# Kernel tuning notes

Hardware: AMD Instinct MI355X
Metric: run time of the kernel (lower is better)

Reference implementation:

```python
import jax, jax.numpy as jnp
import numpy as np

N_NODES = 100000


def gcn_conv(x, W, b, edge_index, n):
    """PyG-style GCNConv: x' = D^-1/2 (A+I) D^-1/2 (x W) + b."""
    loop = jnp.arange(n, dtype=edge_index.dtype)
    src = jnp.concatenate([edge_index[0], loop])
    dst = jnp.concatenate([edge_index[1], loop])
    deg = jax.ops.segment_sum(jnp.ones_like(dst, dtype=x.dtype), dst, num_segments=n)
    dinv = jax.lax.rsqrt(deg)  # deg >= 1 because of self-loops
    norm = dinv[src] * dinv[dst]  # [E+N]
    h = x @ W  # [N, out]
    msg = h[src] * norm[:, None]  # gather + scale
    return jax.ops.segment_sum(msg, dst, num_segments=n) + b


def edge_logits(z, edge_index, We, be):
    # concat(src_emb, dst_emb) @ We + be, without materializing the concat twice
    d = z.shape[1]
    return z[edge_index[0]] @ We[:d] + z[edge_index[1]] @ We[d:] + be


def setup_inputs() -> dict:
    key = jax.random.key(0)
    ks = jax.random.split(key, 10)
    x = jax.random.normal(ks[0], (N_NODES, 512), dtype=jnp.float32)
    edge_index = jax.random.randint(ks[1], (2, 3200000), 0, N_NODES, dtype=jnp.int64)
    pos_edge_index = jax.random.randint(ks[2], (2, 1000000), 0, N_NODES, dtype=jnp.int64)
    neg_edge_index = jax.random.randint(ks[3], (2, 1000000), 0, N_NODES, dtype=jnp.int64)
    s1 = 1.0 / np.sqrt(512)
    s2 = 1.0 / np.sqrt(16)
    se = 1.0 / np.sqrt(128)
    W1 = jax.random.uniform(ks[4], (512, 16), jnp.float32, -s1, s1)
    b1 = jnp.zeros((16,), jnp.float32)
    W2 = jax.random.uniform(ks[5], (16, 64), jnp.float32, -s2, s2)
    b2 = jnp.zeros((64,), jnp.float32)
    We = jax.random.uniform(ks[6], (128, 1), jnp.float32, -se, se)  # 2*num_classes -> 1
    be = jnp.zeros((1,), jnp.float32)
    return {"x": x, "W1": W1, "b1": b1, "W2": W2, "b2": b2, "We": We, "be": be,
            "edge_index": edge_index, "pos_edge_index": pos_edge_index,
            "neg_edge_index": neg_edge_index}


def reference(x, W1, b1, W2, b2, We, be, edge_index, pos_edge_index, neg_edge_index):
    n = x.shape[0]
    h = jax.nn.relu(gcn_conv(x, W1, b1, edge_index, n))
    z = gcn_conv(h, W2, b2, edge_index, n)  # node embeddings [N, num_classes]
    pos = edge_logits(z, pos_edge_index, We, be)
    neg = edge_logits(z, neg_edge_index, We, be)
    return z, jnp.concatenate([pos, neg], axis=0)
```

## Files before the change

kernel.cpp:

```cpp
#include <hip/hip_runtime.h>
#include <hip/hip_bf16.h>
#include <hip/hip_fp16.h>


constexpr int TPB = 256;
constexpr int LOG_W = 7;
constexpr int W_BKT = 128;
constexpr int NB_MAX = 1024;
constexpr int CAP = 5120;
constexpr int EPB = 8192;

__global__ __launch_bounds__(256) void scatterA_kernel(const int* __restrict__ src,
                                                       const int* __restrict__ dst,
                                                       int* __restrict__ bcursor,
                                                       int* __restrict__ pairs,
                                                       int E, int NB) {
    __shared__ int hist[NB_MAX];
    __shared__ int lstart[NB_MAX];
    __shared__ int gbase[NB_MAX];
    __shared__ int lcur[NB_MAX];
    __shared__ int csum[256];
    __shared__ int val[EPB];
    __shared__ unsigned short bkt[EPB];
    const int t = threadIdx.x;
    const int e0 = blockIdx.x * EPB;
    const int cnt = min(EPB, E - e0);

    for (int i = t; i < NB; i += 256) hist[i] = 0;
    __syncthreads();
    for (int i = t; i < cnt; i += 256) atomicAdd(&hist[dst[e0 + i] >> LOG_W], 1);
    __syncthreads();

    int loc[4], tsum = 0;
#pragma unroll
    for (int j = 0; j < 4; ++j) {
        int idx = t * 4 + j;
        int v = (idx < NB) ? hist[idx] : 0;
        loc[j] = tsum; tsum += v;
    }
    csum[t] = tsum;
    __syncthreads();
    for (int off = 1; off < 256; off <<= 1) {
        int v = (t >= off) ? csum[t - off] : 0;
        __syncthreads();
        csum[t] += v;
        __syncthreads();
    }
    int cbase = (t > 0) ? csum[t - 1] : 0;
#pragma unroll
    for (int j = 0; j < 4; ++j) {
        int idx = t * 4 + j;
        if (idx < NB) lstart[idx] = cbase + loc[j];
    }
    __syncthreads();
    for (int b = t; b < NB; b += 256) {
        gbase[b] = hist[b] ? atomicAdd(&bcursor[b], hist[b]) : 0;
        lcur[b] = lstart[b];
    }
    __syncthreads();
    for (int i = t; i < cnt; i += 256) {
        int s = src[e0 + i], d = dst[e0 + i];
        int b = d >> LOG_W;
        int p = atomicAdd(&lcur[b], 1);
        val[p] = ((d & (W_BKT - 1)) << 17) | s;
        bkt[p] = (unsigned short)b;
    }
    __syncthreads();
    for (int i = t; i < cnt; i += 256) {
        int b = bkt[i];
        int ofs = gbase[b] + (i - lstart[b]);
        if (ofs < CAP) pairs[(size_t)b * CAP + ofs] = val[i];
    }
}

__global__ __launch_bounds__(256) void bucketB_kernel(const int* __restrict__ bcursor,
                                                      int* __restrict__ pairs,
                                                      float* __restrict__ dinv,
                                                      int* __restrict__ row_start,
                                                      int* __restrict__ row_end,
                                                      int N) {
    __shared__ int cnt[W_BKT];
    __shared__ int scn[W_BKT];
    __shared__ int cur[W_BKT];
    __shared__ int img[CAP];
    const int b = blockIdx.x;
    const int t = threadIdx.x;
    const int len = min(bcursor[b], CAP);
    const int n0 = b * W_BKT;
    int* p = pairs + (size_t)b * CAP;

    if (t < W_BKT) cnt[t] = 0;
    __syncthreads();
    for (int i = t; i < len; i += 256) atomicAdd(&cnt[p[i] >> 17], 1);
    __syncthreads();
    if (t < W_BKT) scn[t] = cnt[t];
    __syncthreads();
    for (int off = 1; off < W_BKT; off <<= 1) {
        int v = (t < W_BKT && t >= off) ? scn[t - off] : 0;
        __syncthreads();
        if (t < W_BKT) scn[t] += v;
        __syncthreads();
    }
    if (t < W_BKT) {
        int c = cnt[t];
        int es = scn[t] - c;
        cur[t] = es;
        int n = n0 + t;
        if (n < N) {
            dinv[n] = rsqrtf((float)(c + 1));
            int rs = b * CAP + es;
            row_start[n] = rs;
            row_end[n] = rs + c;
        }
    }
    __syncthreads();
    for (int i = t; i < len; i += 256) {
        int v = p[i];
        int r = atomicAdd(&cur[v >> 17], 1);
        img[r] = v & 0x1FFFF;
    }
    __syncthreads();
    for (int i = t; i < len; i += 256) p[i] = img[i];
}

__global__ __launch_bounds__(256) void gemm1_kernel(const float* __restrict__ x,
                                                    const float* __restrict__ W1,
                                                    const float* __restrict__ dinv,
                                                    __half* __restrict__ xs, int N) {
    __shared__ float buf[512 * 16];
    const int t = threadIdx.x;
    {
        const float4* w4 = (const float4*)W1;
        float4* b4 = (float4*)buf;
        for (int i = t; i < 2048; i += 256) b4[i] = w4[i];
    }
    __syncthreads();

    const int r = t & 63, q = t >> 6;
    const int row = blockIdx.x * 64 + r;
    const bool valid = row < N;
    const float* xrow = x + (size_t)row * 512 + q * 128;

    float acc[16];
#pragma unroll
    for (int c = 0; c < 16; ++c) acc[c] = 0.0f;

    if (valid) {
        const int kb = q * 128;
#pragma unroll 2
        for (int k0 = 0; k0 < 128; k0 += 16) {
            const float4* xp = (const float4*)(xrow + k0);
            float4 a0 = xp[0], a1 = xp[1], a2 = xp[2], a3 = xp[3];
            float xv[16] = {a0.x, a0.y, a0.z, a0.w, a1.x, a1.y, a1.z, a1.w,
                            a2.x, a2.y, a2.z, a2.w, a3.x, a3.y, a3.z, a3.w};
#pragma unroll
            for (int kk = 0; kk < 16; ++kk) {
                const float4* wr = (const float4*)(buf + (kb + k0 + kk) * 16);
                float4 w0 = wr[0], w1 = wr[1], w2 = wr[2], w3 = wr[3];
                float xvk = xv[kk];
                acc[0]  += xvk * w0.x; acc[1]  += xvk * w0.y; acc[2]  += xvk * w0.z; acc[3]  += xvk * w0.w;
                acc[4]  += xvk * w1.x; acc[5]  += xvk * w1.y; acc[6]  += xvk * w1.z; acc[7]  += xvk * w1.w;
                acc[8]  += xvk * w2.x; acc[9]  += xvk * w2.y; acc[10] += xvk * w2.z; acc[11] += xvk * w2.w;
                acc[12] += xvk * w3.x; acc[13] += xvk * w3.y; acc[14] += xvk * w3.z; acc[15] += xvk * w3.w;
            }
        }
    }
    __syncthreads();

    float* red = buf;
    if (q > 0) {
        float4* d0 = (float4*)(red + ((q - 1) * 64 + r) * 16);
        d0[0] = make_float4(acc[0], acc[1], acc[2], acc[3]);
        d0[1] = make_float4(acc[4], acc[5], acc[6], acc[7]);
        d0[2] = make_float4(acc[8], acc[9], acc[10], acc[11]);
        d0[3] = make_float4(acc[12], acc[13], acc[14], acc[15]);
    }
    __syncthreads();
    if (q == 0 && valid) {
#pragma unroll
        for (int p = 0; p < 3; ++p) {
            const float* sr = red + (p * 64 + r) * 16;
#pragma unroll
            for (int c = 0; c < 16; ++c) acc[c] += sr[c];
        }
        float di = dinv[row];
        __half hv[16];
#pragma unroll
        for (int c = 0; c < 16; ++c) hv[c] = __float2half_rn(acc[c] * di);
        float4* o = (float4*)(xs + (size_t)row * 16);
        o[0] = *(const float4*)&hv[0];
        o[1] = *(const float4*)&hv[8];
    }
}

__global__ __launch_bounds__(256) void gather1_kernel(const __half* __restrict__ xs,
                                                      const int* __restrict__ csr,
                                                      const int* __restrict__ row_start,
                                                      const int* __restrict__ row_end,
                                                      const float* __restrict__ dinv,
                                                      const float* __restrict__ b1,
                                                      __half* __restrict__ hs, int N) {
    int t = threadIdx.x;
    int node = blockIdx.x * 32 + (t >> 3);
    int l = t & 7;
    if (node >= N) return;
    const __half2* xb = (const __half2*)xs;
    int rs = row_start[node], re = row_end[node];
    float2 f0 = __half22float2(xb[(size_t)node * 8 + l]);
    float ax = f0.x, ay = f0.y;

    int e0 = rs;
    for (; e0 + 8 <= re; e0 += 8) {
        int idx = csr[e0 + l];
        float2 v[8];
#pragma unroll
        for (int j = 0; j < 8; ++j) {
            int s = __shfl(idx, j, 8);
            v[j] = __half22float2(xb[(size_t)s * 8 + l]);
        }
#pragma unroll
        for (int j = 0; j < 8; ++j) { ax += v[j].x; ay += v[j].y; }
    }
    if (e0 < re) {
        int idx = (e0 + l < re) ? csr[e0 + l] : 0;
        int m = re - e0;
        float2 v[8];
#pragma unroll
        for (int j = 0; j < 8; ++j) {
            int s = __shfl(idx, j, 8);
            v[j] = make_float2(0.0f, 0.0f);
            if (j < m) v[j] = __half22float2(xb[(size_t)s * 8 + l]);
        }
#pragma unroll
        for (int j = 0; j < 8; ++j) { ax += v[j].x; ay += v[j].y; }
    }

    float di = dinv[node];
    float2 bb = ((const float2*)b1)[l];
    float h0 = fmaxf(fmaf(di, ax, bb.x), 0.0f) * di;
    float h1 = fmaxf(fmaf(di, ay, bb.y), 0.0f) * di;
    ((__half2*)hs)[(size_t)node * 8 + l] = __floats2half2_rn(h0, h1);
}

__global__ __launch_bounds__(256) void gather2_fin2_kernel(const __half* __restrict__ hs,
                                                           const int* __restrict__ csr,
                                                           const int* __restrict__ row_start,
                                                           const int* __restrict__ row_end,
                                                           const float* __restrict__ dinv,
                                                           const float* __restrict__ W2,
                                                           const float* __restrict__ b2,
                                                           const float* __restrict__ We,
                                                           float* __restrict__ z,
                                                           float* __restrict__ s1,
                                                           float* __restrict__ s2, int N) {
    __shared__ float w2l[16 * 64];
    __shared__ float wel[128];
    __shared__ float b2l[64];
    int t = threadIdx.x;
    for (int i = t; i < 1024; i += 256) w2l[i] = W2[i];
    if (t < 128) wel[t] = We[t];
    if (t < 64) b2l[t] = b2[t];
    __syncthreads();

    int l = t & 7;
    int node = blockIdx.x * 32 + (t >> 3);
    if (node >= N) return;

    const __half2* hb = (const __half2*)hs;
    int rs = row_start[node], re = row_end[node];
    float2 f0 = __half22float2(hb[(size_t)node * 8 + l]);
    float ax = f0.x, ay = f0.y;

    int e0 = rs;
    for (; e0 + 8 <= re; e0 += 8) {
        int idx = csr[e0 + l];
        float2 v[8];
#pragma unroll
        for (int j = 0; j < 8; ++j) {
            int s = __shfl(idx, j, 8);
            v[j] = __half22float2(hb[(size_t)s * 8 + l]);
        }
#pragma unroll
        for (int j = 0; j < 8; ++j) { ax += v[j].x; ay += v[j].y; }
    }
    if (e0 < re) {
        int idx = (e0 + l < re) ? csr[e0 + l] : 0;
        int m = re - e0;
        float2 v[8];
#pragma unroll
        for (int j = 0; j < 8; ++j) {
            int s = __shfl(idx, j, 8);
            v[j] = make_float2(0.0f, 0.0f);
            if (j < m) v[j] = __half22float2(hb[(size_t)s * 8 + l]);
        }
#pragma unroll
        for (int j = 0; j < 8; ++j) { ax += v[j].x; ay += v[j].y; }
    }

    float di = dinv[node];
    float ux = ax * di, uy = ay * di;

    const int c0 = l * 8;
    float zz[8];
#pragma unroll
    for (int cc = 0; cc < 8; ++cc) zz[cc] = b2l[c0 + cc];
#pragma unroll
    for (int k = 0; k < 16; ++k) {
        float uk = __shfl((k & 1) ? uy : ux, k >> 1, 8);
        const float* wr = &w2l[k * 64 + c0];
#pragma unroll
        for (int cc = 0; cc < 8; ++cc) zz[cc] = fmaf(uk, wr[cc], zz[cc]);
    }
    float p1 = 0.0f, p2 = 0.0f;
#pragma unroll
    for (int cc = 0; cc < 8; ++cc) {
        p1 = fmaf(zz[cc], wel[c0 + cc], p1);
        p2 = fmaf(zz[cc], wel[64 + c0 + cc], p2);
    }
#pragma unroll
    for (int off = 1; off < 8; off <<= 1) {
        p1 += __shfl_xor(p1, off, 8);
        p2 += __shfl_xor(p2, off, 8);
    }
    float4* zp = (float4*)(z + (size_t)node * 64 + c0);
    zp[0] = make_float4(zz[0], zz[1], zz[2], zz[3]);
    zp[1] = make_float4(zz[4], zz[5], zz[6], zz[7]);
    if (l == 0) { s1[node] = p1; s2[node] = p2; }
}

__global__ void logits_kernel(const int* __restrict__ psrc, const int* __restrict__ pdst,
                              const int* __restrict__ nsrc, const int* __restrict__ ndst,
                              const float* __restrict__ s1, const float* __restrict__ s2,
                              const float* __restrict__ be, float* __restrict__ out,
                              int EP, int ET) {
    int e = blockIdx.x * blockDim.x + threadIdx.x;
    if (e >= ET) return;
    int s, d;
    if (e < EP) {
        s = psrc[e];
        d = pdst[e];
    } else {
        s = nsrc[e - EP];
        d = ndst[e - EP];
    }
    out[e] = s1[s] + s2[d] + be[0];
}

extern "C" void kernel_launch(void* const* d_in, const int* in_sizes, int n_in,
                              void* d_out, int out_size, void* d_ws, size_t ws_size,
                              hipStream_t stream) {
    const float* x  = (const float*)d_in[0];
    const float* W1 = (const float*)d_in[1];
    const float* b1 = (const float*)d_in[2];
    const float* W2 = (const float*)d_in[3];
    const float* b2 = (const float*)d_in[4];
    const float* We = (const float*)d_in[5];
    const float* be = (const float*)d_in[6];
    const int* ei   = (const int*)d_in[7];
    const int* pei  = (const int*)d_in[8];
    const int* nei  = (const int*)d_in[9];

    const int N  = in_sizes[0] / 512;
    const int E  = in_sizes[7] / 2;
    const int EP = in_sizes[8] / 2;
    const int EN = in_sizes[9] / 2;
    const int NB = (N + W_BKT - 1) >> LOG_W;

    const int* src  = ei;
    const int* dst  = ei + E;
    const int* psrc = pei;
    const int* pdst = pei + EP;
    const int* nsrc = nei;
    const int* ndst = nei + EN;

    int* wsp = (int*)d_ws;
    int*   bcursor   = wsp;
    float* dinv      = (float*)(wsp + NB_MAX);
    int*   row_start = (int*)(dinv + N);
    int*   row_end   = row_start + N;
    float* s1        = (float*)(row_end + N);
    float* s2        = s1 + N;
    __half* xs       = (__half*)(s2 + N);
    __half* hs       = xs + (size_t)16 * N;
    int*   pairs     = (int*)(hs + (size_t)16 * N);

    float* z_out = (float*)d_out;
    float* logit_out = z_out + (size_t)64 * N;

    hipMemsetAsync(bcursor, 0, NB_MAX * sizeof(int), stream);

    int gA  = (E + EPB - 1) / EPB;
    int g32 = (N + 31) / 32;
    int g64 = (N + 63) / 64;

    scatterA_kernel<<<gA, TPB, 0, stream>>>(src, dst, bcursor, pairs, E, NB);
    bucketB_kernel<<<NB, TPB, 0, stream>>>(bcursor, pairs, dinv, row_start, row_end, N);

    gemm1_kernel<<<g64, TPB, 0, stream>>>(x, W1, dinv, xs, N);

    gather1_kernel<<<g32, TPB, 0, stream>>>(xs, pairs, row_start, row_end, dinv, b1, hs, N);
    gather2_fin2_kernel<<<g32, TPB, 0, stream>>>(hs, pairs, row_start, row_end, dinv,
                                                 W2, b2, We, z_out, s1, s2, N);

    int ET = EP + EN;
    int gL = (ET + TPB - 1) / TPB;
    logits_kernel<<<gL, TPB, 0, stream>>>(psrc, pdst, nsrc, ndst, s1, s2, be,
                                          logit_out, EP, ET);
}
```

Before: 465.0 us.

## Co-schedule bucket CSR build with first GEMM in one interleaved launch

```diff
diff --git a/kernel.cpp b/kernel.cpp
--- a/kernel.cpp
+++ b/kernel.cpp
@@ -73,124 +73,141 @@
     }
 }
 
-__global__ __launch_bounds__(256) void bucketB_kernel(const int* __restrict__ bcursor,
-                                                      int* __restrict__ pairs,
-                                                      float* __restrict__ dinv,
-                                                      int* __restrict__ row_start,
-                                                      int* __restrict__ row_end,
-                                                      int N) {
-    __shared__ int cnt[W_BKT];
-    __shared__ int scn[W_BKT];
-    __shared__ int cur[W_BKT];
-    __shared__ int img[CAP];
-    const int b = blockIdx.x;
+__global__ __launch_bounds__(256) void fusedBG_kernel(
+        const int* __restrict__ bcursor,
+        int* __restrict__ pairs,
+        float* __restrict__ dinv,
+        int* __restrict__ row_start,
+        int* __restrict__ row_end,
+        int nB,
+        const float* __restrict__ x,
+        const float* __restrict__ W1,
+        float* __restrict__ xw,
+        int nG, int N) {
+    __shared__ __align__(16) char smem[32768];
     const int t = threadIdx.x;
-    const int len = min(bcursor[b], CAP);
-    const int n0 = b * W_BKT;
-    int* p = pairs + (size_t)b * CAP;
-
-    if (t < W_BKT) cnt[t] = 0;
-    __syncthreads();
-    for (int i = t; i < len; i += 256) atomicAdd(&cnt[p[i] >> 17], 1);
-    __syncthreads();
-    if (t < W_BKT) scn[t] = cnt[t];
-    __syncthreads();
-    for (int off = 1; off < W_BKT; off <<= 1) {
-        int v = (t < W_BKT && t >= off) ? scn[t - off] : 0;
-        __syncthreads();
-        if (t < W_BKT) scn[t] += v;
-        __syncthreads();
-    }
-    if (t < W_BKT) {
-        int c = cnt[t];
-        int es = scn[t] - c;
-        cur[t] = es;
-        int n = n0 + t;
-        if (n < N) {
-            dinv[n] = rsqrtf((float)(c + 1));
-            int rs = b * CAP + es;
-            row_start[n] = rs;
-            row_end[n] = rs + c;
-        }
-    }
-    __syncthreads();
-    for (int i = t; i < len; i += 256) {
-        int v = p[i];
-        int r = atomicAdd(&cur[v >> 17], 1);
-        img[r] = v & 0x1FFFF;
-    }
-    __syncthreads();
-    for (int i = t; i < len; i += 256) p[i] = img[i];
-}
-
-__global__ __launch_bounds__(256) void gemm1_kernel(const float* __restrict__ x,
-                                                    const float* __restrict__ W1,
+    const int bid = blockIdx.x;
+    const int m = min(nB, nG), m2 = 2 * m;
+    int role, idx;
+    if (bid < m2) { role = bid & 1; idx = bid >> 1; }
+    else          { role = (nB > nG) ? 1 : 0; idx = m + (bid - m2); }
+
+    if (role == 1) {
+        int* cnt = (int*)smem;
+        int* scn = cnt + W_BKT;
+        int* cur = scn + W_BKT;
+        int* img = cur + W_BKT;
+        const int b = idx;
+        const int len = min(bcursor[b], CAP);
+        const int n0 = b * W_BKT;
+        int* p = pairs + (size_t)b * CAP;
+
+        if (t < W_BKT) cnt[t] = 0;
+        __syncthreads();
+        for (int i = t; i < len; i += 256) atomicAdd(&cnt[p[i] >> 17], 1);
+        __syncthreads();
+        if (t < W_BKT) scn[t] = cnt[t];
+        __syncthreads();
+        for (int off = 1; off < W_BKT; off <<= 1) {
+            int v = (t < W_BKT && t >= off) ? scn[t - off] : 0;
+            __syncthreads();
+            if (t < W_BKT) scn[t] += v;
+            __syncthreads();
+        }
+        if (t < W_BKT) {
+            int c = cnt[t];
+            int es = scn[t] - c;
+            cur[t] = es;
+            int n = n0 + t;
+            if (n < N) {
+                dinv[n] = rsqrtf((float)(c + 1));
+                int rs = b * CAP + es;
+                row_start[n] = rs;
+                row_end[n] = rs + c;
+            }
+        }
+        __syncthreads();
+        for (int i = t; i < len; i += 256) {
+            int v = p[i];
+            int r = atomicAdd(&cur[v >> 17], 1);
+            img[r] = v & 0x1FFFF;
+        }
+        __syncthreads();
+        for (int i = t; i < len; i += 256) p[i] = img[i];
+    } else {
+        float* buf = (float*)smem;
+        {
+            const float4* w4 = (const float4*)W1;
+            float4* b4 = (float4*)buf;
+            for (int i = t; i < 2048; i += 256) b4[i] = w4[i];
+        }
+        __syncthreads();
+
+        const int r = t & 63, q = t >> 6;
+        const int row = idx * 64 + r;
+        const bool valid = row < N;
+        const float* xrow = x + (size_t)row * 512 + q * 128;
+
+        float acc[16];
+#pragma unroll
+        for (int c = 0; c < 16; ++c) acc[c] = 0.0f;
+
+        if (valid) {
+            const int kb = q * 128;
+#pragma unroll 2
+            for (int k0 = 0; k0 < 128; k0 += 16) {
+                const float4* xp = (const float4*)(xrow + k0);
+                float4 a0 = xp[0], a1 = xp[1], a2 = xp[2], a3 = xp[3];
+                float xv[16] = {a0.x, a0.y, a0.z, a0.w, a1.x, a1.y, a1.z, a1.w,
+                                a2.x, a2.y, a2.z, a2.w, a3.x, a3.y, a3.z, a3.w};
+#pragma unroll
+                for (int kk = 0; kk < 16; ++kk) {
+                    const float4* wr = (const float4*)(buf + (kb + k0 + kk) * 16);
+                    float4 w0 = wr[0], w1 = wr[1], w2 = wr[2], w3 = wr[3];
+                    float xvk = xv[kk];
+                    acc[0]  += xvk * w0.x; acc[1]  += xvk * w0.y; acc[2]  += xvk * w0.z; acc[3]  += xvk * w0.w;
+                    acc[4]  += xvk * w1.x; acc[5]  += xvk * w1.y; acc[6]  += xvk * w1.z; acc[7]  += xvk * w1.w;
+                    acc[8]  += xvk * w2.x; acc[9]  += xvk * w2.y; acc[10] += xvk * w2.z; acc[11] += xvk * w2.w;
+                    acc[12] += xvk * w3.x; acc[13] += xvk * w3.y; acc[14] += xvk * w3.z; acc[15] += xvk * w3.w;
+                }
+            }
+        }
+        __syncthreads();
+
+        float* red = buf;
+        if (q > 0) {
+            float4* d0 = (float4*)(red + ((q - 1) * 64 + r) * 16);
+            d0[0] = make_float4(acc[0], acc[1], acc[2], acc[3]);
+            d0[1] = make_float4(acc[4], acc[5], acc[6], acc[7]);
+            d0[2] = make_float4(acc[8], acc[9], acc[10], acc[11]);
+            d0[3] = make_float4(acc[12], acc[13], acc[14], acc[15]);
+        }
+        __syncthreads();
+        if (q == 0 && valid) {
+#pragma unroll
+            for (int p = 0; p < 3; ++p) {
+                const float* sr = red + (p * 64 + r) * 16;
+#pragma unroll
+                for (int c = 0; c < 16; ++c) acc[c] += sr[c];
+            }
+            float4* o = (float4*)(xw + (size_t)row * 16);
+            o[0] = make_float4(acc[0], acc[1], acc[2], acc[3]);
+            o[1] = make_float4(acc[4], acc[5], acc[6], acc[7]);
+            o[2] = make_float4(acc[8], acc[9], acc[10], acc[11]);
+            o[3] = make_float4(acc[12], acc[13], acc[14], acc[15]);
+        }
+    }
+}
+
+__global__ __launch_bounds__(256) void scale_kernel(const float* __restrict__ xw,
                                                     const float* __restrict__ dinv,
                                                     __half* __restrict__ xs, int N) {
-    __shared__ float buf[512 * 16];
-    const int t = threadIdx.x;
-    {
-        const float4* w4 = (const float4*)W1;
-        float4* b4 = (float4*)buf;
-        for (int i = t; i < 2048; i += 256) b4[i] = w4[i];
-    }
-    __syncthreads();
-
-    const int r = t & 63, q = t >> 6;
-    const int row = blockIdx.x * 64 + r;
-    const bool valid = row < N;
-    const float* xrow = x + (size_t)row * 512 + q * 128;
-
-    float acc[16];
-#pragma unroll
-    for (int c = 0; c < 16; ++c) acc[c] = 0.0f;
-
-    if (valid) {
-        const int kb = q * 128;
-#pragma unroll 2
-        for (int k0 = 0; k0 < 128; k0 += 16) {
-            const float4* xp = (const float4*)(xrow + k0);
-            float4 a0 = xp[0], a1 = xp[1], a2 = xp[2], a3 = xp[3];
-            float xv[16] = {a0.x, a0.y, a0.z, a0.w, a1.x, a1.y, a1.z, a1.w,
-                            a2.x, a2.y, a2.z, a2.w, a3.x, a3.y, a3.z, a3.w};
-#pragma unroll
-            for (int kk = 0; kk < 16; ++kk) {
-                const float4* wr = (const float4*)(buf + (kb + k0 + kk) * 16);
-                float4 w0 = wr[0], w1 = wr[1], w2 = wr[2], w3 = wr[3];
-                float xvk = xv[kk];
-                acc[0]  += xvk * w0.x; acc[1]  += xvk * w0.y; acc[2]  += xvk * w0.z; acc[3]  += xvk * w0.w;
-                acc[4]  += xvk * w1.x; acc[5]  += xvk * w1.y; acc[6]  += xvk * w1.z; acc[7]  += xvk * w1.w;
-                acc[8]  += xvk * w2.x; acc[9]  += xvk * w2.y; acc[10] += xvk * w2.z; acc[11] += xvk * w2.w;
-                acc[12] += xvk * w3.x; acc[13] += xvk * w3.y; acc[14] += xvk * w3.z; acc[15] += xvk * w3.w;
-            }
-        }
-    }
-    __syncthreads();
-
-    float* red = buf;
-    if (q > 0) {
-        float4* d0 = (float4*)(red + ((q - 1) * 64 + r) * 16);
-        d0[0] = make_float4(acc[0], acc[1], acc[2], acc[3]);
-        d0[1] = make_float4(acc[4], acc[5], acc[6], acc[7]);
-        d0[2] = make_float4(acc[8], acc[9], acc[10], acc[11]);
-        d0[3] = make_float4(acc[12], acc[13], acc[14], acc[15]);
-    }
-    __syncthreads();
-    if (q == 0 && valid) {
-#pragma unroll
-        for (int p = 0; p < 3; ++p) {
-            const float* sr = red + (p * 64 + r) * 16;
-#pragma unroll
-            for (int c = 0; c < 16; ++c) acc[c] += sr[c];
-        }
-        float di = dinv[row];
-        __half hv[16];
-#pragma unroll
-        for (int c = 0; c < 16; ++c) hv[c] = __float2half_rn(acc[c] * di);
-        float4* o = (float4*)(xs + (size_t)row * 16);
-        o[0] = *(const float4*)&hv[0];
-        o[1] = *(const float4*)&hv[8];
-    }
+    int i = blockIdx.x * 256 + threadIdx.x;
+    if (i >= N * 8) return;
+    int n = i >> 3, h = i & 7;
+    float di = dinv[n];
+    float2 f = ((const float2*)(xw + (size_t)n * 16))[h];
+    ((__half2*)xs)[i] = __floats2half2_rn(f.x * di, f.y * di);
 }
 
 __global__ __launch_bounds__(256) void gather1_kernel(const __half* __restrict__ xs,
@@ -386,17 +403,22 @@
 
     float* z_out = (float*)d_out;
     float* logit_out = z_out + (size_t)64 * N;
+    float* xw = z_out;
 
     hipMemsetAsync(bcursor, 0, NB_MAX * sizeof(int), stream);
 
     int gA  = (E + EPB - 1) / EPB;
     int g32 = (N + 31) / 32;
-    int g64 = (N + 63) / 64;
+    int gG  = (N + 63) / 64;
 
     scatterA_kernel<<<gA, TPB, 0, stream>>>(src, dst, bcursor, pairs, E, NB);
-    bucketB_kernel<<<NB, TPB, 0, stream>>>(bcursor, pairs, dinv, row_start, row_end, N);
-
-    gemm1_kernel<<<g64, TPB, 0, stream>>>(x, W1, dinv, xs, N);
+
+    fusedBG_kernel<<<NB + gG, TPB, 0, stream>>>(bcursor, pairs, dinv,
+                                                row_start, row_end, NB,
+                                                x, W1, xw, gG, N);
+
+    int gS = (8 * N + TPB - 1) / TPB;
+    scale_kernel<<<gS, TPB, 0, stream>>>(xw, dinv, xs, N);
 
     gather1_kernel<<<g32, TPB, 0, stream>>>(xs, pairs, row_start, row_end, dinv, b1, hs, N);
     gather2_fin2_kernel<<<g32, TPB, 0, stream>>>(hs, pairs, row_start, row_end, dinv,
```

Result: no change. 463.4 us (-0.3%).
